# Optimization experiments

Measured on AMD Instinct MI355X. Metric: run time of the kernel, lower is better.

Reference implementation:

```python
import jax, jax.numpy as jnp
import numpy as np

H = 512      # hidden_size (hardcoded in __init__)
WD = 1024    # word_dim (hardcoded)
V = 4096     # len(i2w)+4
B, S, T = 256, 80, 28


def setup_inputs() -> dict:
    key = jax.random.key(0)
    ks = jax.random.split(key, 14)

    def gl(k, shape, fan_in):
        return (jax.random.normal(k, shape, jnp.float32) / np.sqrt(fan_in)).astype(jnp.float32)

    return {
        "encoder_last_hidden_state": jax.random.normal(ks[0], (1, B, H), jnp.float32),
        "encoder_output": jax.random.normal(ks[1], (B, S, H), jnp.float32),
        "targets": jax.random.randint(ks[2], (B, T), 0, V, dtype=jnp.int32),
        # embedding table
        "embedding": gl(ks[3], (V, WD), WD),
        # attention MLP (4 stacked linears, no activations, per the source)
        "W1": gl(ks[4], (2 * H, H), 2 * H), "b1": jnp.zeros((H,), jnp.float32),
        "W2": gl(ks[5], (H, H), H), "b2": jnp.zeros((H,), jnp.float32),
        "W3": gl(ks[6], (H, H), H), "b3": jnp.zeros((H,), jnp.float32),
        "W4": gl(ks[7], (H, H), H), "b4": jnp.zeros((H,), jnp.float32),
        "Ww": gl(ks[8], (H, 1), H),
        # GRU (input = hidden_size + word_dim = 1536), PyTorch gate order r,z,n
        "W_ih": gl(ks[9], (3 * H, H + WD), H + WD), "b_ih": jnp.zeros((3 * H,), jnp.float32),
        "W_hh": gl(ks[10], (3 * H, H), H), "b_hh": jnp.zeros((3 * H,), jnp.float32),
        # output projection
        "Wo": gl(ks[11], (H, V), H), "bo": jnp.zeros((V,), jnp.float32),
    }


def reference(encoder_last_hidden_state, encoder_output, targets, embedding,
              W1, b1, W2, b2, W3, b3, W4, b4, Ww,
              W_ih, b_ih, W_hh, b_hh, Wo, bo):
    n_steps = targets.shape[1] - 1  # seq_len - 1 decode steps

    def attention(h, enc):
        # h: (B,H) decoder hidden; enc: (B,S,H)
        hs = jnp.broadcast_to(h[:, None, :], enc.shape)
        m = jnp.concatenate([enc, hs], axis=-1)          # (B,S,2H)
        x = m @ W1 + b1
        x = x @ W2 + b2
        x = x @ W3 + b3
        x = x @ W4 + b4
        attw = jax.nn.softmax((x @ Ww)[..., 0], axis=1)  # (B,S)
        return jnp.einsum('bs,bsh->bh', attw, enc)       # context (B,H)

    def gru_cell(x, h):
        gi = x @ W_ih.T + b_ih
        gh = h @ W_hh.T + b_hh
        ir, iz, inn = jnp.split(gi, 3, axis=-1)
        hr, hz, hn = jnp.split(gh, 3, axis=-1)
        r = jax.nn.sigmoid(ir + hr)
        z = jax.nn.sigmoid(iz + hz)
        n = jnp.tanh(inn + r * hn)
        return (1.0 - z) * n + z * h

    h0 = encoder_last_hidden_state[0]                    # (B,H)
    w0 = jnp.ones((encoder_output.shape[0],), jnp.int32) # <BOS> = 1

    def step(carry, _):
        h, w = carry
        emb = embedding[w]                               # (B,WD)
        ctx = attention(h, encoder_output)               # (B,H)
        x = jnp.concatenate([emb, ctx], axis=-1)         # (B,WD+H)
        hn = gru_cell(x, h)
        logits = hn @ Wo + bo                            # (B,V)
        wn = jnp.argmax(logits, axis=-1).astype(jnp.int32)
        return (hn, wn), logits

    _, logits_seq = jax.lax.scan(step, (h0, w0), None, length=n_steps)
    seq_logProb = jnp.swapaxes(logits_seq, 0, 1)         # (B, T-1, V)
    seq_predictions = jnp.argmax(seq_logProb, axis=-1)
    return seq_logProb, seq_predictions
```

## Files before the change

kernel.cpp:

```cpp
#include <hip/hip_runtime.h>

#define B_ 256
#define S_ 80
#define H_ 512
#define V_ 4096
#define NSTEP 27

typedef unsigned short u16;
typedef __attribute__((ext_vector_type(8))) short short8v;
typedef __attribute__((ext_vector_type(4))) float f32x4;
typedef __attribute__((ext_vector_type(4))) unsigned short ushort4v;

#define MFMA_(a,b,c) __builtin_amdgcn_mfma_f32_16x16x32_bf16(a,b,c,0,0,0)
#define MFMA3(acc, ah, al, bh, bl) do{ acc = MFMA_(ah,bh,acc); acc = MFMA_(ah,bl,acc); acc = MFMA_(al,bh,acc);}while(0)

__device__ __forceinline__ unsigned fkey(float v){
    unsigned u = __float_as_uint(v);
    return (u & 0x80000000u) ? ~u : (u | 0x80000000u);
}
__device__ __forceinline__ u16 bf16_rne(float f){
    unsigned u = __float_as_uint(f);
    return (u16)((u + 0x7FFFu + ((u >> 16) & 1u)) >> 16);
}
__device__ __forceinline__ void split_f4(float4 v, ushort4v& hi, ushort4v& lo){
    float arr[4] = {v.x, v.y, v.z, v.w};
    ushort4v h, l;
#pragma unroll
    for (int i = 0; i < 4; ++i){
        u16 hb = bf16_rne(arr[i]);
        h[i] = hb;
        l[i] = bf16_rne(arr[i] - __uint_as_float(((unsigned)hb) << 16));
    }
    hi = h; lo = l;
}

__global__ __launch_bounds__(64) void matvec512(const float* __restrict__ W,
                                                const float* __restrict__ v,
                                                float* __restrict__ out){
    int row = blockIdx.x, lane = threadIdx.x;
    const float* wr = W + row * 512;
    float s = 0.f;
#pragma unroll
    for (int i = 0; i < 8; ++i) s += wr[lane + 64*i] * v[lane + 64*i];
#pragma unroll
    for (int off = 32; off; off >>= 1) s += __shfl_xor(s, off);
    if (lane == 0) out[row] = s;
}

__global__ __launch_bounds__(256) void score_kernel(const float* __restrict__ enc,
                                                    const float* __restrict__ weff,
                                                    float* __restrict__ scores){
    int wv = threadIdx.x >> 6, lane = threadIdx.x & 63;
    int p = blockIdx.x * 4 + wv;
    const float* e = enc + (size_t)p * 512;
    float s = 0.f;
#pragma unroll
    for (int i = 0; i < 8; ++i) s += e[lane + 64*i] * weff[lane + 64*i];
#pragma unroll
    for (int off = 32; off; off >>= 1) s += __shfl_xor(s, off);
    if (lane == 0) scores[p] = s;
}

__global__ __launch_bounds__(512) void softmax_ctx(const float* __restrict__ enc,
                                                   const float* __restrict__ scores,
                                                   float* __restrict__ ctx){
    __shared__ float att[S_];
    int b = blockIdx.x, tid = threadIdx.x;
    if (tid < S_) att[tid] = scores[b*S_ + tid];
    __syncthreads();
    if (tid == 0){
        float mx = att[0];
        for (int s = 1; s < S_; ++s) mx = fmaxf(mx, att[s]);
        float sum = 0.f;
        for (int s = 0; s < S_; ++s){ float e = expf(att[s] - mx); att[s] = e; sum += e; }
        float inv = 1.f / sum;
        for (int s = 0; s < S_; ++s) att[s] *= inv;
    }
    __syncthreads();
    float a = 0.f;
    const float* eb = enc + (size_t)b * (S_*H_);
    for (int s = 0; s < S_; ++s) a += att[s] * eb[s*H_ + tid];
    ctx[b*H_ + tid] = a;
}

template<int TM>
__global__ __launch_bounds__(256) void gemm_abt(const float* __restrict__ A, int lda,
                                                const float* __restrict__ Bm, int ldb,
                                                const float* __restrict__ bias,
                                                float* __restrict__ C, int ldc, int K){
    constexpr int RPT = TM / 16;
    __shared__ float As[16][TM + 4];
    __shared__ float Bs[16][64 + 4];
    int m0 = blockIdx.x * TM, n0 = blockIdx.y * 64;
    int tid = threadIdx.x;
    int lk = tid & 15, lr = tid >> 4;
    int tx = tid & 15, ty = tid >> 4;
    float c[RPT][4] = {};
    for (int k0 = 0; k0 < K; k0 += 16){
#pragma unroll
        for (int i = 0; i < RPT; ++i)
            As[lk][lr*RPT + i] = A[(size_t)(m0 + lr*RPT + i)*lda + k0 + lk];
#pragma unroll
        for (int i = 0; i < 4; ++i)
            Bs[lk][lr*4 + i] = Bm[(size_t)(n0 + lr*4 + i)*ldb + k0 + lk];
        __syncthreads();
#pragma unroll
        for (int k = 0; k < 16; ++k){
            float b4[4];
            *(float4*)b4 = *(const float4*)&Bs[k][tx*4];
#pragma unroll
            for (int i = 0; i < RPT; ++i){
                float a = As[k][ty*RPT + i];
#pragma unroll
                for (int j = 0; j < 4; ++j) c[i][j] += a * b4[j];
            }
        }
        __syncthreads();
    }
#pragma unroll
    for (int j = 0; j < 4; ++j){
        float bb = bias ? bias[n0 + tx*4 + j] : 0.f;
#pragma unroll
        for (int i = 0; i < RPT; ++i)
            C[(size_t)(m0 + ty*RPT + i)*ldc + n0 + tx*4 + j] = c[i][j] + bb;
    }
}

__global__ __launch_bounds__(256) void prep_all(
    const float* __restrict__ Whh, const float* __restrict__ Wo,
    const float* __restrict__ emb, const float* __restrict__ Wih,
    const float* __restrict__ elhs,
    u16* __restrict__ WhhHi, u16* __restrict__ WhhLo,
    u16* __restrict__ WoThi, u16* __restrict__ WoTlo,
    u16* __restrict__ EmbHi, u16* __restrict__ EmbLo,
    u16* __restrict__ WihLHi, u16* __restrict__ WihLLo,
    u16* __restrict__ Sh, u16* __restrict__ Sl,
    unsigned* __restrict__ zp, int nz)
{
    __shared__ float T[64][65];
    int b = blockIdx.x, tid = threadIdx.x;
    if (b < 768){
        int idx = (b*256 + tid)*4;
        float4 v = *(const float4*)&Whh[idx];
        ushort4v h,l; split_f4(v,h,l);
        *(ushort4v*)&WhhHi[idx]=h; *(ushort4v*)&WhhLo[idx]=l;
    } else if (b < 1280){
        int lb = b - 768;
        int k0 = (lb & 7)*64, n0 = (lb >> 3)*64;
#pragma unroll
        for (int i = 0; i < 16; ++i){
            int idx = tid + i*256;
            int kk = idx >> 6, nn = idx & 63;
            T[kk][nn] = Wo[(size_t)(k0+kk)*4096 + n0+nn];
        }
        __syncthreads();
#pragma unroll
        for (int i = 0; i < 16; ++i){
            int idx = tid + i*256;
            int nn = idx >> 6, kk = idx & 63;
            float v = T[kk][nn];
            u16 hi = bf16_rne(v);
            u16 lo = bf16_rne(v - __uint_as_float(((unsigned)hi) << 16));
            size_t o = (size_t)(n0+nn)*512 + k0+kk;
            WoThi[o] = hi; WoTlo[o] = lo;
        }
    } else if (b < 5376){
        int idx = ((b-1280)*256 + tid)*4;
        float4 v = *(const float4*)&emb[idx];
        ushort4v h,l; split_f4(v,h,l);
        *(ushort4v*)&EmbHi[idx]=h; *(ushort4v*)&EmbLo[idx]=l;
    } else if (b < 6912){
        int id = ((b-5376)*256 + tid)*4;
        int r = id >> 10, c = id & 1023;
        float4 v = *(const float4*)&Wih[(size_t)r*1536 + c];
        ushort4v h,l; split_f4(v,h,l);
        *(ushort4v*)&WihLHi[id]=h; *(ushort4v*)&WihLLo[id]=l;
    } else if (b < 7040){
        int idx = ((b-6912)*256 + tid)*4;
        float4 v = *(const float4*)&elhs[idx];
        ushort4v h,l; split_f4(v,h,l);
        *(ushort4v*)&Sh[idx]=h; *(ushort4v*)&Sl[idx]=l;
    } else {
        int i = ((b-7040)*256 + tid)*4;
        if (i < nz){ zp[i]=0u; zp[i+1]=0u; zp[i+2]=0u; zp[i+3]=0u; }
    }
}

__global__ __launch_bounds__(256) void eproj_u16(const u16* __restrict__ Ahi, const u16* __restrict__ Alo,
                                                 const u16* __restrict__ Bhi, const u16* __restrict__ Blo,
                                                 float* __restrict__ C){
    __shared__ u16 Ah[64][40], Al[64][40], Bh[64][40], Bl[64][40];
    int n0 = blockIdx.x * 64, m0 = blockIdx.y * 64;
    int tid = threadIdx.x, lane = tid & 63, wid = tid >> 6;
    int wm = (wid & 1) * 32, wn = (wid >> 1) * 32;
    int l15 = lane & 15, lk = (lane >> 4) * 8;
    f32x4 acc[2][2] = {};
    short8v ra[2], rb[2];
#pragma unroll
    for (int j = 0; j < 2; ++j){
        int c = j*256 + tid;
        int half = c >> 8, i = c & 255, row = i >> 2, k8 = (i & 3)*8;
        ra[j] = *(const short8v*)&(half ? Alo : Ahi)[(size_t)(m0+row)*1024 + k8];
        rb[j] = *(const short8v*)&(half ? Blo : Bhi)[(size_t)(n0+row)*1024 + k8];
    }
    for (int k0 = 0; k0 < 1024; k0 += 32){
        __syncthreads();
#pragma unroll
        for (int j = 0; j < 2; ++j){
            int c = j*256 + tid;
            int half = c >> 8, i = c & 255, row = i >> 2, k8 = (i & 3)*8;
            if (half){ *(short8v*)&Al[row][k8] = ra[j]; *(short8v*)&Bl[row][k8] = rb[j]; }
            else     { *(short8v*)&Ah[row][k8] = ra[j]; *(short8v*)&Bh[row][k8] = rb[j]; }
        }
        __syncthreads();
        if (k0 + 32 < 1024){
#pragma unroll
            for (int j = 0; j < 2; ++j){
                int c = j*256 + tid;
                int half = c >> 8, i = c & 255, row = i >> 2, k8 = (i & 3)*8;
                ra[j] = *(const short8v*)&(half ? Alo : Ahi)[(size_t)(m0+row)*1024 + k0+32 + k8];
                rb[j] = *(const short8v*)&(half ? Blo : Bhi)[(size_t)(n0+row)*1024 + k0+32 + k8];
            }
        }
        short8v ah0 = *(const short8v*)&Ah[wm +  0 + l15][lk];
        short8v ah1 = *(const short8v*)&Ah[wm + 16 + l15][lk];
        short8v al0 = *(const short8v*)&Al[wm +  0 + l15][lk];
        short8v al1 = *(const short8v*)&Al[wm + 16 + l15][lk];
        short8v bh0 = *(const short8v*)&Bh[wn +  0 + l15][lk];
        short8v bh1 = *(const short8v*)&Bh[wn + 16 + l15][lk];
        short8v bl0 = *(const short8v*)&Bl[wn +  0 + l15][lk];
        short8v bl1 = *(const short8v*)&Bl[wn + 16 + l15][lk];
        MFMA3(acc[0][0], ah0, al0, bh0, bl0);
        MFMA3(acc[0][1], ah0, al0, bh1, bl1);
        MFMA3(acc[1][0], ah1, al1, bh0, bl0);
        MFMA3(acc[1][1], ah1, al1, bh1, bl1);
    }
    int col0 = n0 + wn + l15;
    int rg = lane >> 4;
#pragma unroll
    for (int mf = 0; mf < 2; ++mf)
#pragma unroll
        for (int r = 0; r < 4; ++r){
            int row = m0 + wm + mf*16 + rg*4 + r;
            C[(size_t)row*1536 + col0]      = acc[mf][0][r];
            C[(size_t)row*1536 + col0 + 16] = acc[mf][1][r];
        }
}


__global__ __launch_bounds__(256) void gru_pointwise(
    const float* __restrict__ gh, const float* __restrict__ Eproj,
    const float* __restrict__ gictx, const float* __restrict__ bhh,
    const float* __restrict__ hprev, float* __restrict__ hnext,
    u16* __restrict__ Sh, u16* __restrict__ Sl,
    const unsigned long long* __restrict__ Pprev,
    float* __restrict__ preds, int t)
{
    int tid = threadIdx.x;
    int row = blockIdx.x * 2 + (tid >> 7);
    int jj = (tid & 127) * 4;
    int w = 1;
    if (t > 0){
        w = 4095 - (int)(Pprev[row] & 0xFFFFFFFFull);
        if (w < 0) w = 0; if (w > 4095) w = 4095;
        if (jj == 0) preds[row*NSTEP + (t-1)] = (float)w;
    }
    const float* gr = gh + (size_t)row * 1536;
    const float* ep = Eproj + (size_t)w * 1536;
    const float* gc = gictx + (size_t)row * 1536;
    float4 g0 = *(const float4*)&gr[jj];
    float4 g1 = *(const float4*)&gr[512 + jj];
    float4 g2 = *(const float4*)&gr[1024 + jj];
    float4 e0 = *(const float4*)&ep[jj];
    float4 e1 = *(const float4*)&ep[512 + jj];
    float4 e2 = *(const float4*)&ep[1024 + jj];
    float4 c0 = *(const float4*)&gc[jj];
    float4 c1 = *(const float4*)&gc[512 + jj];
    float4 c2 = *(const float4*)&gc[1024 + jj];
    float4 b0 = *(const float4*)&bhh[jj];
    float4 b1 = *(const float4*)&bhh[512 + jj];
    float4 b2 = *(const float4*)&bhh[1024 + jj];
    float4 ho = *(const float4*)&hprev[(size_t)row*512 + jj];
    const float* G0 = (const float*)&g0; const float* G1 = (const float*)&g1;
    const float* G2 = (const float*)&g2;
    const float* E0 = (const float*)&e0; const float* E1 = (const float*)&e1;
    const float* E2 = (const float*)&e2;
    const float* C0 = (const float*)&c0; const float* C1 = (const float*)&c1;
    const float* C2 = (const float*)&c2;
    const float* B0 = (const float*)&b0; const float* B1 = (const float*)&b1;
    const float* B2 = (const float*)&b2;
    const float* HO = (const float*)&ho;
    float4 res;
    float* R = (float*)&res;
#pragma unroll
    for (int i = 0; i < 4; ++i){
        float gir = E0[i] + C0[i] + G0[i] + B0[i];
        float giz = E1[i] + C1[i] + G1[i] + B1[i];
        float gin = E2[i] + C2[i];
        float rr = 1.f / (1.f + expf(-gir));
        float zz = 1.f / (1.f + expf(-giz));
        float nn = tanhf(gin + rr * (G2[i] + B2[i]));
        R[i] = (1.f - zz)*nn + zz*HO[i];
    }
    size_t o = (size_t)row*512 + jj;
    *(float4*)&hnext[o] = res;
    ushort4v h4, l4; split_f4(res, h4, l4);
    *(ushort4v*)&Sh[o] = h4;
    *(ushort4v*)&Sl[o] = l4;
}

__global__ __launch_bounds__(256) void step_mm(
    const u16* __restrict__ Ahg, const u16* __restrict__ Alg,
    const u16* __restrict__ WoHi, const u16* __restrict__ WoLo,
    const u16* __restrict__ WhhHi, const u16* __restrict__ WhhLo,
    const float* __restrict__ bo,
    float* __restrict__ logits, unsigned long long* __restrict__ P,
    float* __restrict__ gh, int n_logits)
{
    __shared__ u16 Ah[64][40], Al[64][40], Bh[128][40], Bl[128][40];
    int m0 = blockIdx.x * 64;
    int nt = blockIdx.y;
    bool isL = nt < n_logits;
    int nbase = (isL ? nt : nt - n_logits) * 128;
    const u16* Bhg = isL ? WoHi : WhhHi;
    const u16* Blg = isL ? WoLo : WhhLo;
    int tid = threadIdx.x, lane = tid & 63, wid = tid >> 6;
    int wy = wid & 1, wx = wid >> 1;
    int l15 = lane & 15, rg = lane >> 4, lk = rg * 8;
    int ar = tid >> 2, ak8 = (tid & 3) * 8;
    const u16* agH = Ahg + (size_t)(m0 + ar)*512 + ak8;
    const u16* agL = Alg + (size_t)(m0 + ar)*512 + ak8;
    const u16* bgH0 = Bhg + (size_t)(nbase + ar)*512 + ak8;
    const u16* bgL0 = Blg + (size_t)(nbase + ar)*512 + ak8;
    const u16* bgH1 = bgH0 + (size_t)64*512;
    const u16* bgL1 = bgL0 + (size_t)64*512;
    f32x4 acc[2][4] = {};
    short8v ra_h = *(const short8v*)agH;
    short8v ra_l = *(const short8v*)agL;
    short8v rb_h0 = *(const short8v*)bgH0;
    short8v rb_l0 = *(const short8v*)bgL0;
    short8v rb_h1 = *(const short8v*)bgH1;
    short8v rb_l1 = *(const short8v*)bgL1;
    for (int k0 = 0; k0 < 512; k0 += 32){
        __syncthreads();
        *(short8v*)&Ah[ar][ak8] = ra_h;
        *(short8v*)&Al[ar][ak8] = ra_l;
        *(short8v*)&Bh[ar][ak8] = rb_h0;
        *(short8v*)&Bl[ar][ak8] = rb_l0;
        *(short8v*)&Bh[64 + ar][ak8] = rb_h1;
        *(short8v*)&Bl[64 + ar][ak8] = rb_l1;
        __syncthreads();
        if (k0 + 32 < 512){
            ra_h  = *(const short8v*)(agH + k0 + 32);
            ra_l  = *(const short8v*)(agL + k0 + 32);
            rb_h0 = *(const short8v*)(bgH0 + k0 + 32);
            rb_l0 = *(const short8v*)(bgL0 + k0 + 32);
            rb_h1 = *(const short8v*)(bgH1 + k0 + 32);
            rb_l1 = *(const short8v*)(bgL1 + k0 + 32);
        }
        short8v af_h[2], af_l[2];
#pragma unroll
        for (int mf = 0; mf < 2; ++mf){
            af_h[mf] = *(const short8v*)&Ah[wy*32 + mf*16 + l15][lk];
            af_l[mf] = *(const short8v*)&Al[wy*32 + mf*16 + l15][lk];
        }
#pragma unroll
        for (int nf = 0; nf < 4; ++nf){
            short8v bfh = *(const short8v*)&Bh[wx*64 + nf*16 + l15][lk];
            short8v bfl = *(const short8v*)&Bl[wx*64 + nf*16 + l15][lk];
            MFMA3(acc[0][nf], af_h[0], af_l[0], bfh, bfl);
            MFMA3(acc[1][nf], af_h[1], af_l[1], bfh, bfl);
        }
    }
    if (isL){
        float bov[4];
#pragma unroll
        for (int nf = 0; nf < 4; ++nf) bov[nf] = bo[nbase + wx*64 + nf*16 + l15];
#pragma unroll
        for (int mf = 0; mf < 2; ++mf){
#pragma unroll
            for (int r = 0; r < 4; ++r){
                int row = m0 + wy*32 + mf*16 + rg*4 + r;
                float* crow = logits + (size_t)row * (NSTEP * (size_t)V_);
                unsigned long long best = 0ULL;
#pragma unroll
                for (int nf = 0; nf < 4; ++nf){
                    int col = nbase + wx*64 + nf*16 + l15;
                    float v = acc[mf][nf][r] + bov[nf];
                    crow[col] = v;
                    unsigned long long key = ((unsigned long long)fkey(v) << 32) | (unsigned)(4095 - col);
                    if (key > best) best = key;
                }
#pragma unroll
                for (int off = 1; off < 16; off <<= 1){
                    unsigned long long o = __shfl_xor(best, off);
                    if (o > best) best = o;
                }
                if (l15 == 0) atomicMax(&P[row], best);
            }
        }
    } else {
#pragma unroll
        for (int mf = 0; mf < 2; ++mf)
#pragma unroll
            for (int nf = 0; nf < 4; ++nf)
#pragma unroll
                for (int r = 0; r < 4; ++r){
                    int row = m0 + wy*32 + mf*16 + rg*4 + r;
                    int col = nbase + wx*64 + nf*16 + l15;
                    gh[(size_t)row*1536 + col] = acc[mf][nf][r];
                }
    }
}

__global__ __launch_bounds__(256) void final_pred(const unsigned long long* __restrict__ P,
                                                  float* __restrict__ preds){
    int b = threadIdx.x;
    int w = 4095 - (int)(P[b] & 0xFFFFFFFFull);
    if (w < 0) w = 0; if (w > 4095) w = 4095;
    preds[b*NSTEP + (NSTEP-1)] = (float)w;
}

extern "C" void kernel_launch(void* const* d_in, const int* in_sizes, int n_in,
                              void* d_out, int out_size, void* d_ws, size_t ws_size,
                              hipStream_t stream){
    const float* elhs = (const float*)d_in[0];
    const float* enc  = (const float*)d_in[1];
    const float* emb  = (const float*)d_in[3];
    const float* W1   = (const float*)d_in[4];
    const float* W2   = (const float*)d_in[6];
    const float* W3   = (const float*)d_in[8];
    const float* W4   = (const float*)d_in[10];
    const float* Ww   = (const float*)d_in[12];
    const float* Wih  = (const float*)d_in[13];
    const float* bih  = (const float*)d_in[14];
    const float* Whh  = (const float*)d_in[15];
    const float* bhh  = (const float*)d_in[16];
    const float* Wo   = (const float*)d_in[17];
    const float* bo   = (const float*)d_in[18];

    float* out = (float*)d_out;
    float* preds = out + (size_t)B_ * NSTEP * V_;

    float* ws = (float*)d_ws;
    float* Eproj  = ws;  ws += (size_t)V_ * 1536;
    float* gictx  = ws;  ws += (size_t)B_ * 1536;
    float* ctx    = ws;  ws += B_ * H_;
    float* scores = ws;  ws += B_ * S_;
    float* t1     = ws;  ws += 512;
    float* t2     = ws;  ws += 512;
    float* weff   = ws;  ws += 512;
    float* Hf     = ws;  ws += 2 * B_ * H_;
    float* ghbuf  = ws;  ws += B_ * 1536;
    u16* WoT_hi = (u16*)ws;  ws += (size_t)V_ * 512 / 2;
    u16* WoT_lo = (u16*)ws;  ws += (size_t)V_ * 512 / 2;
    u16* WhhHi  = (u16*)ws;  ws += 1536 * 512 / 2;
    u16* WhhLo  = (u16*)ws;  ws += 1536 * 512 / 2;
    u16* Sh     = (u16*)ws;  ws += B_ * H_ / 2;
    u16* Sl     = (u16*)ws;  ws += B_ * H_ / 2;
    unsigned long long* P = (unsigned long long*)ws;

    u16* EmbHi  = (u16*)d_out;
    u16* EmbLo  = EmbHi + (size_t)V_*1024;
    u16* WihLHi = EmbLo + (size_t)V_*1024;
    u16* WihLLo = WihLHi + (size_t)1536*1024;

    prep_all<<<7054, 256, 0, stream>>>(Whh, Wo, emb, Wih, elhs,
                                       WhhHi, WhhLo, WoT_hi, WoT_lo,
                                       EmbHi, EmbLo, WihLHi, WihLLo,
                                       Sh, Sl, (unsigned*)P, NSTEP*256*2);

    matvec512<<<512, 64, 0, stream>>>(W4, Ww, t1);
    matvec512<<<512, 64, 0, stream>>>(W3, t1, t2);
    matvec512<<<512, 64, 0, stream>>>(W2, t2, t1);
    matvec512<<<512, 64, 0, stream>>>(W1, t1, weff);
    score_kernel<<<(B_*S_)/4, 256, 0, stream>>>(enc, weff, scores);
    softmax_ctx<<<B_, 512, 0, stream>>>(enc, scores, ctx);
    { dim3 g(B_/32, 1536/64);
      gemm_abt<32><<<g, 256, 0, stream>>>(ctx, 512, Wih + 1024, 1536, bih, gictx, 1536, 512); }
    { dim3 g(1536/64, V_/64);
      eproj_u16<<<g, 256, 0, stream>>>(EmbHi, EmbLo, WihLHi, WihLLo, Eproj); }

    { dim3 g(4, 12);
      step_mm<<<g, 256, 0, stream>>>(Sh, Sl, WoT_hi, WoT_lo, WhhHi, WhhLo, bo,
                                     out, P, ghbuf, 0); }

    for (int t = 0; t < NSTEP; ++t){
        const float* hr = (t == 0) ? elhs : (Hf + (size_t)((t-1) & 1) * (B_*H_));
        float* hw = Hf + (size_t)(t & 1) * (B_*H_);
        const unsigned long long* Pprev = P + (size_t)(t > 0 ? t-1 : 0) * 256;
        gru_pointwise<<<128, 256, 0, stream>>>(ghbuf, Eproj, gictx, bhh, hr, hw,
                                               Sh, Sl, Pprev, preds, t);
        dim3 g(4, 32 + 12);
        step_mm<<<g, 256, 0, stream>>>(Sh, Sl, WoT_hi, WoT_lo, WhhHi, WhhLo, bo,
                                       out + (size_t)t * V_, P + (size_t)t*256, ghbuf, 32);
    }
    final_pred<<<1, 256, 0, stream>>>(P + (size_t)(NSTEP-1)*256, preds);
}
```

Measured before the change: 778.3 us.

## Fuse GRU pointwise update into step GEMM prologue with double-buffered gh

The separate gru_pointwise kernel is removed. Each step_mm block now recomputes the GRU cell update for its 64 rows, one K-slice at a time, and feeds the new hidden state straight into shared memory as the A operand, instead of reading Sh/Sl written by a prior kernel. This halves the per-step launch count and removes a global round trip for the bf16-split hidden state. The cost is that the pointwise math is done redundantly across all 44 column tiles. The gh buffer becomes double-buffered to avoid a read/write race, and the LDS row padding changes from 40 to 44.

```diff
diff --git a/kernel.cpp b/kernel.cpp
--- a/kernel.cpp
+++ b/kernel.cpp
@@ -189,7 +189,7 @@
 __global__ __launch_bounds__(256) void eproj_u16(const u16* __restrict__ Ahi, const u16* __restrict__ Alo,
                                                  const u16* __restrict__ Bhi, const u16* __restrict__ Blo,
                                                  float* __restrict__ C){
-    __shared__ u16 Ah[64][40], Al[64][40], Bh[64][40], Bl[64][40];
+    __shared__ u16 Ah[64][44], Al[64][44], Bh[64][44], Bl[64][44];
     int n0 = blockIdx.x * 64, m0 = blockIdx.y * 64;
     int tid = threadIdx.x, lane = tid & 63, wid = tid >> 6;
     int wm = (wid & 1) * 32, wn = (wid >> 1) * 32;
@@ -247,77 +247,22 @@
         }
 }
 
-
-__global__ __launch_bounds__(256) void gru_pointwise(
+template<bool FUSE>
+__global__ __launch_bounds__(256) void step_mm(
+    const u16* __restrict__ Ahg, const u16* __restrict__ Alg,
     const float* __restrict__ gh, const float* __restrict__ Eproj,
     const float* __restrict__ gictx, const float* __restrict__ bhh,
     const float* __restrict__ hprev, float* __restrict__ hnext,
-    u16* __restrict__ Sh, u16* __restrict__ Sl,
-    const unsigned long long* __restrict__ Pprev,
-    float* __restrict__ preds, int t)
-{
-    int tid = threadIdx.x;
-    int row = blockIdx.x * 2 + (tid >> 7);
-    int jj = (tid & 127) * 4;
-    int w = 1;
-    if (t > 0){
-        w = 4095 - (int)(Pprev[row] & 0xFFFFFFFFull);
-        if (w < 0) w = 0; if (w > 4095) w = 4095;
-        if (jj == 0) preds[row*NSTEP + (t-1)] = (float)w;
-    }
-    const float* gr = gh + (size_t)row * 1536;
-    const float* ep = Eproj + (size_t)w * 1536;
-    const float* gc = gictx + (size_t)row * 1536;
-    float4 g0 = *(const float4*)&gr[jj];
-    float4 g1 = *(const float4*)&gr[512 + jj];
-    float4 g2 = *(const float4*)&gr[1024 + jj];
-    float4 e0 = *(const float4*)&ep[jj];
-    float4 e1 = *(const float4*)&ep[512 + jj];
-    float4 e2 = *(const float4*)&ep[1024 + jj];
-    float4 c0 = *(const float4*)&gc[jj];
-    float4 c1 = *(const float4*)&gc[512 + jj];
-    float4 c2 = *(const float4*)&gc[1024 + jj];
-    float4 b0 = *(const float4*)&bhh[jj];
-    float4 b1 = *(const float4*)&bhh[512 + jj];
-    float4 b2 = *(const float4*)&bhh[1024 + jj];
-    float4 ho = *(const float4*)&hprev[(size_t)row*512 + jj];
-    const float* G0 = (const float*)&g0; const float* G1 = (const float*)&g1;
-    const float* G2 = (const float*)&g2;
-    const float* E0 = (const float*)&e0; const float* E1 = (const float*)&e1;
-    const float* E2 = (const float*)&e2;
-    const float* C0 = (const float*)&c0; const float* C1 = (const float*)&c1;
-    const float* C2 = (const float*)&c2;
-    const float* B0 = (const float*)&b0; const float* B1 = (const float*)&b1;
-    const float* B2 = (const float*)&b2;
-    const float* HO = (const float*)&ho;
-    float4 res;
-    float* R = (float*)&res;
-#pragma unroll
-    for (int i = 0; i < 4; ++i){
-        float gir = E0[i] + C0[i] + G0[i] + B0[i];
-        float giz = E1[i] + C1[i] + G1[i] + B1[i];
-        float gin = E2[i] + C2[i];
-        float rr = 1.f / (1.f + expf(-gir));
-        float zz = 1.f / (1.f + expf(-giz));
-        float nn = tanhf(gin + rr * (G2[i] + B2[i]));
-        R[i] = (1.f - zz)*nn + zz*HO[i];
-    }
-    size_t o = (size_t)row*512 + jj;
-    *(float4*)&hnext[o] = res;
-    ushort4v h4, l4; split_f4(res, h4, l4);
-    *(ushort4v*)&Sh[o] = h4;
-    *(ushort4v*)&Sl[o] = l4;
-}
-
-__global__ __launch_bounds__(256) void step_mm(
-    const u16* __restrict__ Ahg, const u16* __restrict__ Alg,
     const u16* __restrict__ WoHi, const u16* __restrict__ WoLo,
     const u16* __restrict__ WhhHi, const u16* __restrict__ WhhLo,
     const float* __restrict__ bo,
-    float* __restrict__ logits, unsigned long long* __restrict__ P,
-    float* __restrict__ gh, int n_logits)
+    float* __restrict__ logits, unsigned long long* __restrict__ Pcur,
+    const unsigned long long* __restrict__ Pprev,
+    float* __restrict__ gh_out, float* __restrict__ preds,
+    int n_logits, int t)
 {
-    __shared__ u16 Ah[64][40], Al[64][40], Bh[128][40], Bl[128][40];
+    __shared__ u16 Ah[64][44], Al[64][44], Bh[128][44], Bl[128][44];
+    __shared__ int widx[64];
     int m0 = blockIdx.x * 64;
     int nt = blockIdx.y;
     bool isL = nt < n_logits;
@@ -328,31 +273,116 @@
     int wy = wid & 1, wx = wid >> 1;
     int l15 = lane & 15, rg = lane >> 4, lk = rg * 8;
     int ar = tid >> 2, ak8 = (tid & 3) * 8;
+
+    if (FUSE){
+        if (tid < 64){
+            int b = m0 + tid;
+            int w = 1;
+            if (t > 0){
+                w = 4095 - (int)(Pprev[b] & 0xFFFFFFFFull);
+                if (w < 0) w = 0; if (w > 4095) w = 4095;
+                if (nt == 0) preds[b*NSTEP + (t-1)] = (float)w;
+            }
+            widx[tid] = w;
+        }
+        __syncthreads();
+    }
+
     const u16* agH = Ahg + (size_t)(m0 + ar)*512 + ak8;
     const u16* agL = Alg + (size_t)(m0 + ar)*512 + ak8;
     const u16* bgH0 = Bhg + (size_t)(nbase + ar)*512 + ak8;
     const u16* bgL0 = Blg + (size_t)(nbase + ar)*512 + ak8;
     const u16* bgH1 = bgH0 + (size_t)64*512;
     const u16* bgL1 = bgL0 + (size_t)64*512;
-    f32x4 acc[2][4] = {};
-    short8v ra_h = *(const short8v*)agH;
-    short8v ra_l = *(const short8v*)agL;
+
+    int wrow = FUSE ? widx[ar] : 0;
+    const int grow = m0 + ar;
+    const float* grp = gh + (size_t)grow * 1536;
+    const float* epp = Eproj + (size_t)wrow * 1536;
+    const float* gcp = gictx + (size_t)grow * 1536;
+
+    ushort4v hnH0, hnH1, hnL0, hnL1;
+    short8v ra_h, ra_l;
+
+#define GRU_SLICE(K0) do{                                                     \
+    int j = (K0) + ak8;                                                       \
+    float G[8], E[8], Cc[8], Bb[8], G2[8], E2[8], C2[8], B2[8];               \
+    float G1[8], E1[8], C1[8], B1[8], HP[8], R[8];                            \
+    *(float4*)&G[0]  = *(const float4*)&grp[j];                               \
+    *(float4*)&G[4]  = *(const float4*)&grp[j+4];                             \
+    *(float4*)&G1[0] = *(const float4*)&grp[512+j];                           \
+    *(float4*)&G1[4] = *(const float4*)&grp[512+j+4];                         \
+    *(float4*)&G2[0] = *(const float4*)&grp[1024+j];                          \
+    *(float4*)&G2[4] = *(const float4*)&grp[1024+j+4];                        \
+    *(float4*)&E[0]  = *(const float4*)&epp[j];                               \
+    *(float4*)&E[4]  = *(const float4*)&epp[j+4];                             \
+    *(float4*)&E1[0] = *(const float4*)&epp[512+j];                           \
+    *(float4*)&E1[4] = *(const float4*)&epp[512+j+4];                         \
+    *(float4*)&E2[0] = *(const float4*)&epp[1024+j];                          \
+    *(float4*)&E2[4] = *(const float4*)&epp[1024+j+4];                        \
+    *(float4*)&Cc[0] = *(const float4*)&gcp[j];                               \
+    *(float4*)&Cc[4] = *(const float4*)&gcp[j+4];                             \
+    *(float4*)&C1[0] = *(const float4*)&gcp[512+j];                           \
+    *(float4*)&C1[4] = *(const float4*)&gcp[512+j+4];                         \
+    *(float4*)&C2[0] = *(const float4*)&gcp[1024+j];                          \
+    *(float4*)&C2[4] = *(const float4*)&gcp[1024+j+4];                        \
+    *(float4*)&Bb[0] = *(const float4*)&bhh[j];                               \
+    *(float4*)&Bb[4] = *(const float4*)&bhh[j+4];                             \
+    *(float4*)&B1[0] = *(const float4*)&bhh[512+j];                           \
+    *(float4*)&B1[4] = *(const float4*)&bhh[512+j+4];                         \
+    *(float4*)&B2[0] = *(const float4*)&bhh[1024+j];                          \
+    *(float4*)&B2[4] = *(const float4*)&bhh[1024+j+4];                        \
+    *(float4*)&HP[0] = *(const float4*)&hprev[(size_t)grow*512 + j];          \
+    *(float4*)&HP[4] = *(const float4*)&hprev[(size_t)grow*512 + j+4];        \
+    _Pragma("unroll")                                                         \
+    for (int i = 0; i < 8; ++i){                                              \
+        float gir = E[i] + Cc[i] + G[i] + Bb[i];                              \
+        float giz = E1[i] + C1[i] + G1[i] + B1[i];                            \
+        float gin = E2[i] + C2[i];                                            \
+        float rr = 1.f / (1.f + expf(-gir));                                  \
+        float zz = 1.f / (1.f + expf(-giz));                                  \
+        float nn = tanhf(gin + rr * (G2[i] + B2[i]));                         \
+        R[i] = (1.f - zz)*nn + zz*HP[i];                                      \
+    }                                                                         \
+    if (nt == 0){                                                             \
+        *(float4*)&hnext[(size_t)grow*512 + j]   = *(float4*)&R[0];           \
+        *(float4*)&hnext[(size_t)grow*512 + j+4] = *(float4*)&R[4];           \
+    }                                                                         \
+    split_f4(*(float4*)&R[0], hnH0, hnL0);                                    \
+    split_f4(*(float4*)&R[4], hnH1, hnL1);                                    \
+}while(0)
+
+    if (FUSE) GRU_SLICE(0);
+    else { ra_h = *(const short8v*)agH; ra_l = *(const short8v*)agL; }
+
     short8v rb_h0 = *(const short8v*)bgH0;
     short8v rb_l0 = *(const short8v*)bgL0;
     short8v rb_h1 = *(const short8v*)bgH1;
     short8v rb_l1 = *(const short8v*)bgL1;
+    f32x4 acc[2][4] = {};
+
     for (int k0 = 0; k0 < 512; k0 += 32){
         __syncthreads();
-        *(short8v*)&Ah[ar][ak8] = ra_h;
-        *(short8v*)&Al[ar][ak8] = ra_l;
+        if (FUSE){
+            *(ushort4v*)&Ah[ar][ak8]   = hnH0;
+            *(ushort4v*)&Ah[ar][ak8+4] = hnH1;
+            *(ushort4v*)&Al[ar][ak8]   = hnL0;
+            *(ushort4v*)&Al[ar][ak8+4] = hnL1;
+        } else {
+            *(short8v*)&Ah[ar][ak8] = ra_h;
+            *(short8v*)&Al[ar][ak8] = ra_l;
+        }
         *(short8v*)&Bh[ar][ak8] = rb_h0;
         *(short8v*)&Bl[ar][ak8] = rb_l0;
         *(short8v*)&Bh[64 + ar][ak8] = rb_h1;
         *(short8v*)&Bl[64 + ar][ak8] = rb_l1;
         __syncthreads();
         if (k0 + 32 < 512){
-            ra_h  = *(const short8v*)(agH + k0 + 32);
-            ra_l  = *(const short8v*)(agL + k0 + 32);
+            if (FUSE) GRU_SLICE(k0 + 32);
+            else {
+                ra_h = *(const short8v*)(agH + k0 + 32);
+                ra_l = *(const short8v*)(agL + k0 + 32);
+            }
             rb_h0 = *(const short8v*)(bgH0 + k0 + 32);
             rb_l0 = *(const short8v*)(bgL0 + k0 + 32);
             rb_h1 = *(const short8v*)(bgH1 + k0 + 32);
@@ -396,7 +426,7 @@
                     unsigned long long o = __shfl_xor(best, off);
                     if (o > best) best = o;
                 }
-                if (l15 == 0) atomicMax(&P[row], best);
+                if (l15 == 0) atomicMax(&Pcur[row], best);
             }
         }
     } else {
@@ -408,7 +438,7 @@
                 for (int r = 0; r < 4; ++r){
                     int row = m0 + wy*32 + mf*16 + rg*4 + r;
                     int col = nbase + wx*64 + nf*16 + l15;
-                    gh[(size_t)row*1536 + col] = acc[mf][nf][r];
+                    gh_out[(size_t)row*1536 + col] = acc[mf][nf][r];
                 }
     }
 }
@@ -451,7 +481,8 @@
     float* t2     = ws;  ws += 512;
     float* weff   = ws;  ws += 512;
     float* Hf     = ws;  ws += 2 * B_ * H_;
-    float* ghbuf  = ws;  ws += B_ * 1536;
+    float* ghA    = ws;  ws += B_ * 1536;
+    float* ghB    = ws;  ws += B_ * 1536;
     u16* WoT_hi = (u16*)ws;  ws += (size_t)V_ * 512 / 2;
     u16* WoT_lo = (u16*)ws;  ws += (size_t)V_ * 512 / 2;
     u16* WhhHi  = (u16*)ws;  ws += 1536 * 512 / 2;
@@ -482,18 +513,23 @@
       eproj_u16<<<g, 256, 0, stream>>>(EmbHi, EmbLo, WihLHi, WihLLo, Eproj); }
 
     { dim3 g(4, 12);
-      step_mm<<<g, 256, 0, stream>>>(Sh, Sl, WoT_hi, WoT_lo, WhhHi, WhhLo, bo,
-                                     out, P, ghbuf, 0); }
+      step_mm<false><<<g, 256, 0, stream>>>(Sh, Sl,
+          nullptr, nullptr, nullptr, nullptr, nullptr, nullptr,
+          WoT_hi, WoT_lo, WhhHi, WhhLo, bo,
+          out, P, P, ghA, preds, 0, 0); }
 
     for (int t = 0; t < NSTEP; ++t){
+        const float* gh_in  = (t & 1) ? ghB : ghA;
+        float*       gh_nx  = (t & 1) ? ghA : ghB;
         const float* hr = (t == 0) ? elhs : (Hf + (size_t)((t-1) & 1) * (B_*H_));
-        float* hw = Hf + (size_t)(t & 1) * (B_*H_);
-        const unsigned long long* Pprev = P + (size_t)(t > 0 ? t-1 : 0) * 256;
-        gru_pointwise<<<128, 256, 0, stream>>>(ghbuf, Eproj, gictx, bhh, hr, hw,
-                                               Sh, Sl, Pprev, preds, t);
+        float*       hw = Hf + (size_t)(t & 1) * (B_*H_);
         dim3 g(4, 32 + 12);
-        step_mm<<<g, 256, 0, stream>>>(Sh, Sl, WoT_hi, WoT_lo, WhhHi, WhhLo, bo,
-                                       out + (size_t)t * V_, P + (size_t)t*256, ghbuf, 32);
+        step_mm<true><<<g, 256, 0, stream>>>(Sh, Sl,
+            gh_in, Eproj, gictx, bhh, hr, hw,
+            WoT_hi, WoT_lo, WhhHi, WhhLo, bo,
+            out + (size_t)t * V_, P + (size_t)t*256,
+            (t > 0) ? (P + (size_t)(t-1)*256) : P,
+            gh_nx, preds, 32, t);
     }
     final_pred<<<1, 256, 0, stream>>>(P + (size_t)(NSTEP-1)*256, preds);
 }
```

Measured after the change: 1.653 ms. +112.4%, slower.

## Shrink step_mm tile to 64x64, load A fragments directly from global

Applied to the files above, without the earlier changes.

The per-step GEMM kernel now uses 64-column output tiles instead of 128, which doubles the grid (4x88 blocks) to fill more of the GPU's compute units. A-operand fragments are loaded straight from global memory into registers in MFMA layout instead of being staged through shared memory. LDS row padding changes from 40 to 44 elements to reduce bank conflicts, in both step_mm and eproj_u16. The trade-off is less reuse per block, more global reads of the hidden state (served from L2), and twice as many atomicMax operations on the argmax buffer.

```diff
diff --git a/kernel.cpp b/kernel.cpp
--- a/kernel.cpp
+++ b/kernel.cpp
@@ -189,7 +189,7 @@
 __global__ __launch_bounds__(256) void eproj_u16(const u16* __restrict__ Ahi, const u16* __restrict__ Alo,
                                                  const u16* __restrict__ Bhi, const u16* __restrict__ Blo,
                                                  float* __restrict__ C){
-    __shared__ u16 Ah[64][40], Al[64][40], Bh[64][40], Bl[64][40];
+    __shared__ u16 Ah[64][44], Al[64][44], Bh[64][44], Bl[64][44];
     int n0 = blockIdx.x * 64, m0 = blockIdx.y * 64;
     int tid = threadIdx.x, lane = tid & 63, wid = tid >> 6;
     int wm = (wid & 1) * 32, wn = (wid >> 1) * 32;
@@ -314,102 +314,96 @@
     const u16* __restrict__ WoHi, const u16* __restrict__ WoLo,
     const u16* __restrict__ WhhHi, const u16* __restrict__ WhhLo,
     const float* __restrict__ bo,
-    float* __restrict__ logits, unsigned long long* __restrict__ P,
-    float* __restrict__ gh, int n_logits)
+    float* __restrict__ logits, unsigned long long* __restrict__ Pcur,
+    float* __restrict__ gh_out, int n_logits)
 {
-    __shared__ u16 Ah[64][40], Al[64][40], Bh[128][40], Bl[128][40];
+    __shared__ u16 Bh[64][44], Bl[64][44];
     int m0 = blockIdx.x * 64;
     int nt = blockIdx.y;
     bool isL = nt < n_logits;
-    int nbase = (isL ? nt : nt - n_logits) * 128;
+    int nbase = (isL ? nt : nt - n_logits) * 64;
     const u16* Bhg = isL ? WoHi : WhhHi;
     const u16* Blg = isL ? WoLo : WhhLo;
     int tid = threadIdx.x, lane = tid & 63, wid = tid >> 6;
     int wy = wid & 1, wx = wid >> 1;
     int l15 = lane & 15, rg = lane >> 4, lk = rg * 8;
     int ar = tid >> 2, ak8 = (tid & 3) * 8;
-    const u16* agH = Ahg + (size_t)(m0 + ar)*512 + ak8;
-    const u16* agL = Alg + (size_t)(m0 + ar)*512 + ak8;
-    const u16* bgH0 = Bhg + (size_t)(nbase + ar)*512 + ak8;
-    const u16* bgL0 = Blg + (size_t)(nbase + ar)*512 + ak8;
-    const u16* bgH1 = bgH0 + (size_t)64*512;
-    const u16* bgL1 = bgL0 + (size_t)64*512;
-    f32x4 acc[2][4] = {};
-    short8v ra_h = *(const short8v*)agH;
-    short8v ra_l = *(const short8v*)agL;
-    short8v rb_h0 = *(const short8v*)bgH0;
-    short8v rb_l0 = *(const short8v*)bgL0;
-    short8v rb_h1 = *(const short8v*)bgH1;
-    short8v rb_l1 = *(const short8v*)bgL1;
+
+    const u16* bgH = Bhg + (size_t)(nbase + ar)*512 + ak8;
+    const u16* bgL = Blg + (size_t)(nbase + ar)*512 + ak8;
+    const u16* agH0 = Ahg + (size_t)(m0 + wy*32 +  0 + l15)*512 + lk;
+    const u16* agH1 = Ahg + (size_t)(m0 + wy*32 + 16 + l15)*512 + lk;
+    const u16* agL0 = Alg + (size_t)(m0 + wy*32 +  0 + l15)*512 + lk;
+    const u16* agL1 = Alg + (size_t)(m0 + wy*32 + 16 + l15)*512 + lk;
+
+    f32x4 acc[2][2] = {};
+    short8v rb_h = *(const short8v*)bgH;
+    short8v rb_l = *(const short8v*)bgL;
+    short8v ah0 = *(const short8v*)agH0;
+    short8v ah1 = *(const short8v*)agH1;
+    short8v al0 = *(const short8v*)agL0;
+    short8v al1 = *(const short8v*)agL1;
+
     for (int k0 = 0; k0 < 512; k0 += 32){
         __syncthreads();
-        *(short8v*)&Ah[ar][ak8] = ra_h;
-        *(short8v*)&Al[ar][ak8] = ra_l;
-        *(short8v*)&Bh[ar][ak8] = rb_h0;
-        *(short8v*)&Bl[ar][ak8] = rb_l0;
-        *(short8v*)&Bh[64 + ar][ak8] = rb_h1;
-        *(short8v*)&Bl[64 + ar][ak8] = rb_l1;
-        __syncthreads();
+        *(short8v*)&Bh[ar][ak8] = rb_h;
+        *(short8v*)&Bl[ar][ak8] = rb_l;
+        __syncthreads();
+        short8v nah0, nah1, nal0, nal1;
         if (k0 + 32 < 512){
-            ra_h  = *(const short8v*)(agH + k0 + 32);
-            ra_l  = *(const short8v*)(agL + k0 + 32);
-            rb_h0 = *(const short8v*)(bgH0 + k0 + 32);
-            rb_l0 = *(const short8v*)(bgL0 + k0 + 32);
-            rb_h1 = *(const short8v*)(bgH1 + k0 + 32);
-            rb_l1 = *(const short8v*)(bgL1 + k0 + 32);
-        }
-        short8v af_h[2], af_l[2];
-#pragma unroll
-        for (int mf = 0; mf < 2; ++mf){
-            af_h[mf] = *(const short8v*)&Ah[wy*32 + mf*16 + l15][lk];
-            af_l[mf] = *(const short8v*)&Al[wy*32 + mf*16 + l15][lk];
-        }
-#pragma unroll
-        for (int nf = 0; nf < 4; ++nf){
-            short8v bfh = *(const short8v*)&Bh[wx*64 + nf*16 + l15][lk];
-            short8v bfl = *(const short8v*)&Bl[wx*64 + nf*16 + l15][lk];
-            MFMA3(acc[0][nf], af_h[0], af_l[0], bfh, bfl);
-            MFMA3(acc[1][nf], af_h[1], af_l[1], bfh, bfl);
+            rb_h = *(const short8v*)(bgH + k0 + 32);
+            rb_l = *(const short8v*)(bgL + k0 + 32);
+            nah0 = *(const short8v*)(agH0 + k0 + 32);
+            nah1 = *(const short8v*)(agH1 + k0 + 32);
+            nal0 = *(const short8v*)(agL0 + k0 + 32);
+            nal1 = *(const short8v*)(agL1 + k0 + 32);
+        }
+        short8v bh0 = *(const short8v*)&Bh[wx*32 +  0 + l15][lk];
+        short8v bh1 = *(const short8v*)&Bh[wx*32 + 16 + l15][lk];
+        short8v bl0 = *(const short8v*)&Bl[wx*32 +  0 + l15][lk];
+        short8v bl1 = *(const short8v*)&Bl[wx*32 + 16 + l15][lk];
+        MFMA3(acc[0][0], ah0, al0, bh0, bl0);
+        MFMA3(acc[0][1], ah0, al0, bh1, bl1);
+        MFMA3(acc[1][0], ah1, al1, bh0, bl0);
+        MFMA3(acc[1][1], ah1, al1, bh1, bl1);
+        if (k0 + 32 < 512){
+            ah0 = nah0; ah1 = nah1; al0 = nal0; al1 = nal1;
         }
     }
     if (isL){
-        float bov[4];
-#pragma unroll
-        for (int nf = 0; nf < 4; ++nf) bov[nf] = bo[nbase + wx*64 + nf*16 + l15];
+        int col0 = nbase + wx*32 + l15;
+        float bo0 = bo[col0], bo1 = bo[col0 + 16];
 #pragma unroll
         for (int mf = 0; mf < 2; ++mf){
 #pragma unroll
             for (int r = 0; r < 4; ++r){
                 int row = m0 + wy*32 + mf*16 + rg*4 + r;
+                float v0 = acc[mf][0][r] + bo0;
+                float v1 = acc[mf][1][r] + bo1;
                 float* crow = logits + (size_t)row * (NSTEP * (size_t)V_);
-                unsigned long long best = 0ULL;
-#pragma unroll
-                for (int nf = 0; nf < 4; ++nf){
-                    int col = nbase + wx*64 + nf*16 + l15;
-                    float v = acc[mf][nf][r] + bov[nf];
-                    crow[col] = v;
-                    unsigned long long key = ((unsigned long long)fkey(v) << 32) | (unsigned)(4095 - col);
-                    if (key > best) best = key;
-                }
+                crow[col0]      = v0;
+                crow[col0 + 16] = v1;
+                unsigned long long k0_ = ((unsigned long long)fkey(v0) << 32) | (unsigned)(4095 - col0);
+                unsigned long long k1_ = ((unsigned long long)fkey(v1) << 32) | (unsigned)(4095 - (col0+16));
+                unsigned long long best = k0_ > k1_ ? k0_ : k1_;
 #pragma unroll
                 for (int off = 1; off < 16; off <<= 1){
                     unsigned long long o = __shfl_xor(best, off);
                     if (o > best) best = o;
                 }
-                if (l15 == 0) atomicMax(&P[row], best);
+                if (l15 == 0) atomicMax(&Pcur[row], best);
             }
         }
     } else {
+        int col0 = nbase + wx*32 + l15;
 #pragma unroll
         for (int mf = 0; mf < 2; ++mf)
 #pragma unroll
-            for (int nf = 0; nf < 4; ++nf)
-#pragma unroll
-                for (int r = 0; r < 4; ++r){
-                    int row = m0 + wy*32 + mf*16 + rg*4 + r;
-                    int col = nbase + wx*64 + nf*16 + l15;
-                    gh[(size_t)row*1536 + col] = acc[mf][nf][r];
-                }
+            for (int r = 0; r < 4; ++r){
+                int row = m0 + wy*32 + mf*16 + rg*4 + r;
+                gh_out[(size_t)row*1536 + col0]      = acc[mf][0][r];
+                gh_out[(size_t)row*1536 + col0 + 16] = acc[mf][1][r];
+            }
     }
 }
 
@@ -481,19 +475,19 @@
     { dim3 g(1536/64, V_/64);
       eproj_u16<<<g, 256, 0, stream>>>(EmbHi, EmbLo, WihLHi, WihLLo, Eproj); }
 
-    { dim3 g(4, 12);
+    { dim3 g(4, 24);
       step_mm<<<g, 256, 0, stream>>>(Sh, Sl, WoT_hi, WoT_lo, WhhHi, WhhLo, bo,
                                      out, P, ghbuf, 0); }
 
     for (int t = 0; t < NSTEP; ++t){
         const float* hr = (t == 0) ? elhs : (Hf + (size_t)((t-1) & 1) * (B_*H_));
-        float* hw = Hf + (size_t)(t & 1) * (B_*H_);
+        float*       hw = Hf + (size_t)(t & 1) * (B_*H_);
         const unsigned long long* Pprev = P + (size_t)(t > 0 ? t-1 : 0) * 256;
         gru_pointwise<<<128, 256, 0, stream>>>(ghbuf, Eproj, gictx, bhh, hr, hw,
                                                Sh, Sl, Pprev, preds, t);
-        dim3 g(4, 32 + 12);
+        dim3 g(4, 64 + 24);
         step_mm<<<g, 256, 0, stream>>>(Sh, Sl, WoT_hi, WoT_lo, WhhHi, WhhLo, bo,
-                                       out + (size_t)t * V_, P + (size_t)t*256, ghbuf, 32);
+                                       out + (size_t)t * V_, P + (size_t)t*256, ghbuf, 64);
     }
     final_pred<<<1, 256, 0, stream>>>(P + (size_t)(NSTEP-1)*256, preds);
 }
```

Measured after the change: 938.2 us. 1.21x slower.
